# Kernel tuning notes

Hardware: AMD Instinct MI355X
Metric: run time of the kernel (lower is better)

Reference implementation:

```python
import jax, jax.numpy as jnp
import numpy as np

B, S, IN, H, C = 4, 1024, 1024, 256, 8

def setup_inputs() -> dict:
    key = jax.random.key(0)
    ks = jax.random.split(key, 9)
    scale_in = 1.0 / np.sqrt(IN)
    scale_h2 = 1.0 / np.sqrt(2 * H)
    return {
        "seq_feats": jax.random.normal(ks[0], (B, S, IN), dtype=jnp.float32),
        "U": jax.random.normal(ks[1], (H, C, H), dtype=jnp.float32) * 0.02,
        "W_weight": jax.random.uniform(ks[2], (C, 2 * H), minval=-scale_h2, maxval=scale_h2, dtype=jnp.float32),
        "W_bias": jax.random.uniform(ks[3], (C,), minval=-scale_h2, maxval=scale_h2, dtype=jnp.float32),
        "start_w": jax.random.uniform(ks[4], (H, IN), minval=-scale_in, maxval=scale_in, dtype=jnp.float32),
        "start_b": jax.random.uniform(ks[5], (H,), minval=-scale_in, maxval=scale_in, dtype=jnp.float32),
        "end_w": jax.random.uniform(ks[6], (H, IN), minval=-scale_in, maxval=scale_in, dtype=jnp.float32),
        "end_b": jax.random.uniform(ks[7], (H,), minval=-scale_in, maxval=scale_in, dtype=jnp.float32),
    }

def reference(seq_feats, U, W_weight, W_bias, start_w, start_b, end_w, end_b):
    # Hs, He: [b, s, h]
    Hs = jnp.einsum('bsi,hi->bsh', seq_feats, start_w) + start_b
    He = jnp.einsum('bsi,hi->bsh', seq_feats, end_w) + end_b
    # biaffine: [b, s, e, c]
    biaff = jnp.einsum('bsh,hcg,beg->bsec', Hs, U, He)
    # Linear over concat([Hs_repeat, He_repeat]) == split-weight broadcast sum
    Ws, We = W_weight[:, :256], W_weight[:, 256:]
    lin = (jnp.einsum('bsh,ch->bsc', Hs, Ws)[:, :, None, :]
           + jnp.einsum('beh,ch->bec', He, We)[:, None, :, :]
           + W_bias)
    return biaff + lin
```

## Files before the change

### kernel.cpp

```cpp
#include <hip/hip_runtime.h>
#include <stdint.h>


#define BDIM 256

typedef float f32x4 __attribute__((ext_vector_type(4)));
typedef __bf16 bf16x8 __attribute__((ext_vector_type(8)));
typedef unsigned int u32;
typedef unsigned short u16;
typedef const __attribute__((address_space(1))) u32* gas_ptr;
typedef __attribute__((address_space(3))) u32* las_ptr;

static __device__ __forceinline__ void load_lds16(const void* g, void* l) {
  __builtin_amdgcn_global_load_lds((gas_ptr)g, (las_ptr)l, 16, 0, 0);
}

static __device__ __forceinline__ u16 f32_to_bf16(float f) {
  union { float f; u32 u; } v; v.f = f;
  u32 r = v.u + 0x7FFFu + ((v.u >> 16) & 1u);
  return (u16)(r >> 16);
}
static __device__ __forceinline__ float bf16lo_to_f32(u32 u) {
  union { u32 u; float f; } v; v.u = u << 16;
  return v.f;
}
static __device__ __forceinline__ float bf16hi_to_f32(u32 u) {
  union { u32 u; float f; } v; v.u = u & 0xFFFF0000u;
  return v.f;
}

static __device__ __forceinline__ void stage32(u16* lds, int dst, const u16* src,
                                               int srow, int ld, int kcol, int tid) {
  const int r = tid >> 3;
  const int sl = tid & 7;
  load_lds16(src + (size_t)(srow + r) * ld + kcol + ((sl ^ (r & 7)) << 3),
             &lds[dst + tid * 8]);
}

static __device__ __forceinline__ bf16x8 rd64(const u16* lds, int base, int row, int kslot) {
  return *reinterpret_cast<const bf16x8*>(&lds[base + row * 64 + ((kslot ^ (row & 7)) << 3)]);
}

__global__ __launch_bounds__(BDIM, 4)
void k1(const u16* __restrict__ Xbf,
        const u16* __restrict__ wbf,
        u16* __restrict__ Hboth,
        const float* __restrict__ sb,
        const float* __restrict__ eb)
{
  __shared__ u16 lds[2 * 4096];

  const int tid  = threadIdx.x;
  const int lane = tid & 63;
  const int wv   = tid >> 6;
  const int wr   = wv >> 1;
  const int wq   = wv & 1;
  const int rA   = lane & 15;
  const int kq   = lane >> 4;

  int id = blockIdx.y * gridDim.x + blockIdx.x;
  id = (id & 7) * 64 + (id >> 3);
  const int n0 = (id & 7) * 64;
  const int m0 = (id >> 3) * 64;

  f32x4 acc[2][2];
#pragma unroll
  for (int i = 0; i < 2; ++i)
#pragma unroll
    for (int j = 0; j < 2; ++j) acc[i][j] = (f32x4)0.f;

#pragma unroll 1
  for (int kt = 0; kt < 1024; kt += 64) {
    stage32(lds, 0,        Xbf, m0,      1024, kt, tid);
    stage32(lds, 2048,     Xbf, m0 + 32, 1024, kt, tid);
    stage32(lds, 4096,     wbf, n0,      1024, kt, tid);
    stage32(lds, 4096+2048,wbf, n0 + 32, 1024, kt, tid);
    __syncthreads();

    bf16x8 aF[2][2], bF[2][2];
#pragma unroll
    for (int mi = 0; mi < 2; ++mi)
#pragma unroll
      for (int ks = 0; ks < 2; ++ks)
        aF[mi][ks] = rd64(lds, 0, wr * 32 + mi * 16 + rA, (ks << 2) | kq);
#pragma unroll
    for (int ni = 0; ni < 2; ++ni)
#pragma unroll
      for (int ks = 0; ks < 2; ++ks)
        bF[ni][ks] = rd64(lds, 4096, wq * 32 + ni * 16 + rA, (ks << 2) | kq);
#pragma unroll
    for (int mi = 0; mi < 2; ++mi)
#pragma unroll
      for (int ni = 0; ni < 2; ++ni)
#pragma unroll
        for (int ks = 0; ks < 2; ++ks)
          acc[mi][ni] = __builtin_amdgcn_mfma_f32_16x16x32_bf16(
              aF[mi][ks], bF[ni][ks], acc[mi][ni], 0, 0, 0);
    __syncthreads();
  }

#pragma unroll
  for (int mi = 0; mi < 2; ++mi) {
#pragma unroll
    for (int ni = 0; ni < 2; ++ni) {
      const int n = n0 + wq * 32 + ni * 16 + rA;
      const float bn = (n < 256) ? sb[n] : eb[n - 256];
      const int mr = m0 + wr * 32 + mi * 16 + kq * 4;
#pragma unroll
      for (int r = 0; r < 4; ++r)
        Hboth[(size_t)(mr + r) * 512 + n] = f32_to_bf16(acc[mi][ni][r] + bn);
    }
  }
}

__global__ __launch_bounds__(BDIM, 4)
void gemm128_biaff(const u16* __restrict__ Tall,
                   const u16* __restrict__ Bg,
                   float* __restrict__ Out,
                   const float* __restrict__ linSall,
                   const float* __restrict__ linEall)
{
  __shared__ u16 lds[2 * 8192];

  const int tid  = threadIdx.x;
  const int lane = tid & 63;
  const int wv   = tid >> 6;
  const int wr   = wv >> 1;
  const int wc   = wv & 1;
  const int rA   = lane & 15;
  const int kq   = lane >> 4;
  const int z    = blockIdx.z;

  int id = blockIdx.y * gridDim.x + blockIdx.x;
  id = (id & 7) * 64 + (id >> 3);
  const int n0 = (id & 7) * 128;
  const int m0 = (id >> 3) * 128;

  const u16* Ag  = Tall + (size_t)z * (8192 * 256);
  const u16* Bgz = Bg   + (size_t)z * (1024 * 512);

  f32x4 acc[4][4];
#pragma unroll
  for (int i = 0; i < 4; ++i)
#pragma unroll
    for (int j = 0; j < 4; ++j) acc[i][j] = (f32x4)0.f;

#pragma unroll 1
  for (int kt = 0; kt < 256; kt += 64) {
#pragma unroll
    for (int h = 0; h < 4; ++h)
      stage32(lds, h * 2048, Ag, m0 + h * 32, 256, kt, tid);
#pragma unroll
    for (int h = 0; h < 4; ++h)
      stage32(lds, 8192 + h * 2048, Bgz, n0 + h * 32, 512, kt, tid);
    __syncthreads();

    bf16x8 aF[4][2], bF[4][2];
#pragma unroll
    for (int mi = 0; mi < 4; ++mi)
#pragma unroll
      for (int ks = 0; ks < 2; ++ks)
        aF[mi][ks] = rd64(lds, 0, wr * 64 + mi * 16 + rA, (ks << 2) | kq);
#pragma unroll
    for (int ni = 0; ni < 4; ++ni)
#pragma unroll
      for (int ks = 0; ks < 2; ++ks)
        bF[ni][ks] = rd64(lds, 8192, wc * 64 + ni * 16 + rA, (ks << 2) | kq);
#pragma unroll
    for (int mi = 0; mi < 4; ++mi)
#pragma unroll
      for (int ni = 0; ni < 4; ++ni)
#pragma unroll
        for (int ks = 0; ks < 2; ++ks)
          acc[mi][ni] = __builtin_amdgcn_mfma_f32_16x16x32_bf16(
              aF[mi][ks], bF[ni][ks], acc[mi][ni], 0, 0, 0);
    __syncthreads();
  }

  float* OutZ = Out + (size_t)z * 8388608;
  const float* lS = linSall + (size_t)z * 8192;
  const float* lE = linEall + (size_t)z * 8192;
#pragma unroll
  for (int mi = 0; mi < 4; ++mi) {
#pragma unroll
    for (int ni = 0; ni < 4; ++ni) {
      const int mBase = m0 + wr * 64 + mi * 16 + kq * 4;
      const int e = n0 + wc * 64 + ni * 16 + rA;
      const int s = mBase >> 3;
      const int c0 = mBase & 7;
      const float4 ls4 = *reinterpret_cast<const float4*>(lS + mBase);
      const float4 le4 = *reinterpret_cast<const float4*>(lE + (e << 3) + c0);
      float4 o;
      o.x = acc[mi][ni][0] + ls4.x + le4.x;
      o.y = acc[mi][ni][1] + ls4.y + le4.y;
      o.z = acc[mi][ni][2] + ls4.z + le4.z;
      o.w = acc[mi][ni][3] + ls4.w + le4.w;
      *reinterpret_cast<float4*>(OutZ + ((size_t)s << 13) + ((size_t)e << 3) + c0) = o;
    }
  }
}

__global__ __launch_bounds__(BDIM, 2)
void k2lin(const u16* __restrict__ Hboth,
           const u16* __restrict__ Utbf,
           u16* __restrict__ Tbf,
           const float* __restrict__ Ww,
           const float* __restrict__ Wb,
           float* __restrict__ linS,
           float* __restrict__ linE)
{
  const int bid = blockIdx.x;
  const int tid = threadIdx.x;

  if (bid >= 512) {
    const int idx = (bid - 512) * BDIM + tid;
    const int m = idx >> 3;
    const int c = idx & 7;
    const uint4* hs4 = reinterpret_cast<const uint4*>(Hboth + (size_t)m * 512);
    const uint4* he4 = reinterpret_cast<const uint4*>(Hboth + (size_t)m * 512 + 256);
    const float* wsp = Ww + c * 512;
    const float* wep = wsp + 256;
    float s1 = 0.f, s2 = 0.f;
#pragma unroll 4
    for (int t = 0; t < 32; ++t) {
      const uint4 a = hs4[t];
      const uint4 b = he4[t];
      const u32 aw[4] = {a.x, a.y, a.z, a.w};
      const u32 bw[4] = {b.x, b.y, b.z, b.w};
#pragma unroll
      for (int q = 0; q < 4; ++q) {
        const int h = t * 8 + q * 2;
        s1 += bf16lo_to_f32(aw[q]) * wsp[h] + bf16hi_to_f32(aw[q]) * wsp[h + 1];
        s2 += bf16lo_to_f32(bw[q]) * wep[h] + bf16hi_to_f32(bw[q]) * wep[h + 1];
      }
    }
    linS[idx] = s1;
    linE[idx] = s2 + Wb[c];
    return;
  }

  __shared__ u16 lsA[128 * 32];
  __shared__ u16 lsB[128 * 32];

  int id = bid;
  id = (id & 7) * 64 + (id >> 3);
  const int n0 = (id & 15) * 128;
  const int m0 = (id >> 4) * 128;

  const int lane = tid & 63;
  const int wv   = tid >> 6;
  const int wr   = wv >> 1;
  const int wc   = wv & 1;
  const int rA   = lane & 15;
  const int ko   = (lane >> 4) * 8;

  f32x4 acc[4][4];
#pragma unroll
  for (int i = 0; i < 4; ++i)
#pragma unroll
    for (int j = 0; j < 4; ++j) acc[i][j] = (f32x4)0.f;

  for (int kt = 0; kt < 256; kt += 32) {
#pragma unroll
    for (int it = 0; it < 2; ++it) {
      const int chunk = it * BDIM + tid;
      const int row = chunk >> 2;
      const int ce = (chunk & 3) * 8;
      load_lds16(Hboth + (size_t)(m0 + row) * 512 + (kt + ce), &lsA[chunk * 8]);
      load_lds16(Utbf + (size_t)(n0 + row) * 256 + (kt + ce), &lsB[chunk * 8]);
    }
    __syncthreads();

    bf16x8 aF[4], bF[4];
#pragma unroll
    for (int i = 0; i < 4; ++i)
      aF[i] = *reinterpret_cast<const bf16x8*>(&lsA[(wr * 64 + i * 16 + rA) * 32 + ko]);
#pragma unroll
    for (int j = 0; j < 4; ++j)
      bF[j] = *reinterpret_cast<const bf16x8*>(&lsB[(wc * 64 + j * 16 + rA) * 32 + ko]);
#pragma unroll
    for (int i = 0; i < 4; ++i)
#pragma unroll
      for (int j = 0; j < 4; ++j)
        acc[i][j] = __builtin_amdgcn_mfma_f32_16x16x32_bf16(aF[i], bF[j], acc[i][j], 0, 0, 0);
    __syncthreads();
  }

  const int rgr = (lane >> 4) * 4;
#pragma unroll
  for (int i = 0; i < 4; ++i) {
#pragma unroll
    for (int j = 0; j < 4; ++j) {
      const int mBase = m0 + wr * 64 + i * 16 + rgr;
      const int n = n0 + wc * 64 + j * 16 + rA;
#pragma unroll
      for (int r = 0; r < 4; ++r)
        Tbf[(size_t)(mBase + r) * 2048 + n] = f32_to_bf16(acc[i][j][r]);
    }
  }
}

__global__ void prep_kernel(const float* __restrict__ seq,
                            const float* __restrict__ sw,
                            const float* __restrict__ ew,
                            const float* __restrict__ U,
                            u16* __restrict__ Xbf,
                            u16* __restrict__ wbf,
                            u16* __restrict__ Ut)
{
  const int bid = blockIdx.x;
  const int tid = threadIdx.x;
  if (bid < 4096) {
    const int i = bid * 1024 + tid * 4;
    const float4 v = *reinterpret_cast<const float4*>(seq + i);
    ushort4 o;
    o.x = f32_to_bf16(v.x); o.y = f32_to_bf16(v.y);
    o.z = f32_to_bf16(v.z); o.w = f32_to_bf16(v.w);
    *reinterpret_cast<ushort4*>(Xbf + i) = o;
  } else if (bid < 4608) {
    const int i = (bid - 4096) * 1024 + tid * 4;
    const float* src = (i < 262144) ? (sw + i) : (ew + (i - 262144));
    const float4 v = *reinterpret_cast<const float4*>(src);
    ushort4 o;
    o.x = f32_to_bf16(v.x); o.y = f32_to_bf16(v.y);
    o.z = f32_to_bf16(v.z); o.w = f32_to_bf16(v.w);
    *reinterpret_cast<ushort4*>(wbf + i) = o;
  } else {
    const int i = (bid - 4608) * 1024 + tid * 4;
    const int n = i >> 8;
    const int h = i & 255;
    ushort4 o;
    o.x = f32_to_bf16(U[(size_t)(h + 0) * 2048 + n]);
    o.y = f32_to_bf16(U[(size_t)(h + 1) * 2048 + n]);
    o.z = f32_to_bf16(U[(size_t)(h + 2) * 2048 + n]);
    o.w = f32_to_bf16(U[(size_t)(h + 3) * 2048 + n]);
    *reinterpret_cast<ushort4*>(Ut + i) = o;
  }
}

extern "C" void kernel_launch(void* const* d_in, const int* in_sizes, int n_in,
                              void* d_out, int out_size, void* d_ws, size_t ws_size,
                              hipStream_t stream)
{
  const float* seq = (const float*)d_in[0];
  const float* U   = (const float*)d_in[1];
  const float* Ww  = (const float*)d_in[2];
  const float* Wb  = (const float*)d_in[3];
  const float* sw  = (const float*)d_in[4];
  const float* sb  = (const float*)d_in[5];
  const float* ew  = (const float*)d_in[6];
  const float* eb  = (const float*)d_in[7];
  float* out = (float*)d_out;

  u16* Xbf   = (u16*)d_ws;
  u16* wbf   = Xbf  + 4194304;
  u16* Utbf  = wbf  + 524288;
  u16* Hboth = Utbf + 524288;
  u16* Tbf   = Hboth + 2097152;
  float* linS = (float*)(Tbf + 8388608);
  float* linE = linS + 32768;

  prep_kernel<<<5120, BDIM, 0, stream>>>(seq, sw, ew, U, Xbf, wbf, Utbf);

  k1<<<dim3(8, 64, 1), BDIM, 0, stream>>>(Xbf, wbf, Hboth, sb, eb);

  k2lin<<<640, BDIM, 0, stream>>>(Hboth, Utbf, Tbf, Ww, Wb, linS, linE);

  gemm128_biaff<<<dim3(8, 64, 4), BDIM, 0, stream>>>(
      Tbf, Hboth + 256, out, linS, linE);
}
```

Baseline: 85.19 us.

## Fuse fp32-to-bf16 conversion into projection GEMM and restage k2 tiles

Removes the separate prep kernel. The projection GEMM now reads fp32 seq and weights directly, converting them to bf16 as it stages them into LDS, and the U transpose runs in extra blocks of the same launch. The biaffine intermediate GEMM in k2lin switches to 64-wide K tiles with the swizzled LDS layout. This saves a full write and re-read of the bf16 copy of seq plus one launch. In exchange, the staging path now uses synchronous register loads plus conversion instead of asynchronous global-to-LDS loads, and each block re-reads fp32 data at twice the byte count.

```diff
diff --git a/kernel.cpp b/kernel.cpp
--- a/kernel.cpp
+++ b/kernel.cpp
@@ -20,6 +20,9 @@
   u32 r = v.u + 0x7FFFu + ((v.u >> 16) & 1u);
   return (u16)(r >> 16);
 }
+static __device__ __forceinline__ u32 pack_bf16(float lo, float hi) {
+  return (u32)f32_to_bf16(lo) | ((u32)f32_to_bf16(hi) << 16);
+}
 static __device__ __forceinline__ float bf16lo_to_f32(u32 u) {
   union { u32 u; float f; } v; v.u = u << 16;
   return v.f;
@@ -37,20 +40,53 @@
              &lds[dst + tid * 8]);
 }
 
+static __device__ __forceinline__ void stage32_f32(u16* lds, int dst, const float* src,
+                                                   int srow, int ld, int kcol, int tid) {
+  const int r = tid >> 3;
+  const int sl = tid & 7;
+  const float* p = src + (size_t)(srow + r) * ld + kcol + ((sl ^ (r & 7)) << 3);
+  const float4 v0 = *reinterpret_cast<const float4*>(p);
+  const float4 v1 = *reinterpret_cast<const float4*>(p + 4);
+  uint4 w;
+  w.x = pack_bf16(v0.x, v0.y);
+  w.y = pack_bf16(v0.z, v0.w);
+  w.z = pack_bf16(v1.x, v1.y);
+  w.w = pack_bf16(v1.z, v1.w);
+  *reinterpret_cast<uint4*>(&lds[dst + tid * 8]) = w;
+}
+
 static __device__ __forceinline__ bf16x8 rd64(const u16* lds, int base, int row, int kslot) {
   return *reinterpret_cast<const bf16x8*>(&lds[base + row * 64 + ((kslot ^ (row & 7)) << 3)]);
 }
 
 __global__ __launch_bounds__(BDIM, 4)
-void k1(const u16* __restrict__ Xbf,
-        const u16* __restrict__ wbf,
-        u16* __restrict__ Hboth,
-        const float* __restrict__ sb,
-        const float* __restrict__ eb)
+void k1p(const float* __restrict__ seq,
+         const float* __restrict__ sw,
+         const float* __restrict__ ew,
+         const float* __restrict__ U,
+         const float* __restrict__ sb,
+         const float* __restrict__ eb,
+         u16* __restrict__ Hboth,
+         u16* __restrict__ Ut)
 {
+  const int tid = threadIdx.x;
+  const int bid = blockIdx.x;
+
+  if (bid >= 512) {
+    const int i = (bid - 512) * 1024 + tid * 4;
+    const int n = i >> 8;
+    const int h = i & 255;
+    ushort4 o;
+    o.x = f32_to_bf16(U[(size_t)(h + 0) * 2048 + n]);
+    o.y = f32_to_bf16(U[(size_t)(h + 1) * 2048 + n]);
+    o.z = f32_to_bf16(U[(size_t)(h + 2) * 2048 + n]);
+    o.w = f32_to_bf16(U[(size_t)(h + 3) * 2048 + n]);
+    *reinterpret_cast<ushort4*>(Ut + i) = o;
+    return;
+  }
+
   __shared__ u16 lds[2 * 4096];
 
-  const int tid  = threadIdx.x;
   const int lane = tid & 63;
   const int wv   = tid >> 6;
   const int wr   = wv >> 1;
@@ -58,11 +94,14 @@
   const int rA   = lane & 15;
   const int kq   = lane >> 4;
 
-  int id = blockIdx.y * gridDim.x + blockIdx.x;
+  int id = bid;
   id = (id & 7) * 64 + (id >> 3);
   const int n0 = (id & 7) * 64;
   const int m0 = (id >> 3) * 64;
 
+  const float* wsrc = (n0 < 256) ? (sw + (size_t)n0 * 1024)
+                                 : (ew + (size_t)(n0 - 256) * 1024);
+
   f32x4 acc[2][2];
 #pragma unroll
   for (int i = 0; i < 2; ++i)
@@ -71,10 +110,10 @@
 
 #pragma unroll 1
   for (int kt = 0; kt < 1024; kt += 64) {
-    stage32(lds, 0,        Xbf, m0,      1024, kt, tid);
-    stage32(lds, 2048,     Xbf, m0 + 32, 1024, kt, tid);
-    stage32(lds, 4096,     wbf, n0,      1024, kt, tid);
-    stage32(lds, 4096+2048,wbf, n0 + 32, 1024, kt, tid);
+    stage32_f32(lds, 0,           seq,  m0,      1024, kt, tid);
+    stage32_f32(lds, 2048,        seq,  m0 + 32, 1024, kt, tid);
+    stage32_f32(lds, 4096,        wsrc, 0,       1024, kt, tid);
+    stage32_f32(lds, 4096 + 2048, wsrc, 32,      1024, kt, tid);
     __syncthreads();
 
     bf16x8 aF[2][2], bF[2][2];
@@ -109,93 +148,6 @@
 #pragma unroll
       for (int r = 0; r < 4; ++r)
         Hboth[(size_t)(mr + r) * 512 + n] = f32_to_bf16(acc[mi][ni][r] + bn);
-    }
-  }
-}
-
-__global__ __launch_bounds__(BDIM, 4)
-void gemm128_biaff(const u16* __restrict__ Tall,
-                   const u16* __restrict__ Bg,
-                   float* __restrict__ Out,
-                   const float* __restrict__ linSall,
-                   const float* __restrict__ linEall)
-{
-  __shared__ u16 lds[2 * 8192];
-
-  const int tid  = threadIdx.x;
-  const int lane = tid & 63;
-  const int wv   = tid >> 6;
-  const int wr   = wv >> 1;
-  const int wc   = wv & 1;
-  const int rA   = lane & 15;
-  const int kq   = lane >> 4;
-  const int z    = blockIdx.z;
-
-  int id = blockIdx.y * gridDim.x + blockIdx.x;
-  id = (id & 7) * 64 + (id >> 3);
-  const int n0 = (id & 7) * 128;
-  const int m0 = (id >> 3) * 128;
-
-  const u16* Ag  = Tall + (size_t)z * (8192 * 256);
-  const u16* Bgz = Bg   + (size_t)z * (1024 * 512);
-
-  f32x4 acc[4][4];
-#pragma unroll
-  for (int i = 0; i < 4; ++i)
-#pragma unroll
-    for (int j = 0; j < 4; ++j) acc[i][j] = (f32x4)0.f;
-
-#pragma unroll 1
-  for (int kt = 0; kt < 256; kt += 64) {
-#pragma unroll
-    for (int h = 0; h < 4; ++h)
-      stage32(lds, h * 2048, Ag, m0 + h * 32, 256, kt, tid);
-#pragma unroll
-    for (int h = 0; h < 4; ++h)
-      stage32(lds, 8192 + h * 2048, Bgz, n0 + h * 32, 512, kt, tid);
-    __syncthreads();
-
-    bf16x8 aF[4][2], bF[4][2];
-#pragma unroll
-    for (int mi = 0; mi < 4; ++mi)
-#pragma unroll
-      for (int ks = 0; ks < 2; ++ks)
-        aF[mi][ks] = rd64(lds, 0, wr * 64 + mi * 16 + rA, (ks << 2) | kq);
-#pragma unroll
-    for (int ni = 0; ni < 4; ++ni)
-#pragma unroll
-      for (int ks = 0; ks < 2; ++ks)
-        bF[ni][ks] = rd64(lds, 8192, wc * 64 + ni * 16 + rA, (ks << 2) | kq);
-#pragma unroll
-    for (int mi = 0; mi < 4; ++mi)
-#pragma unroll
-      for (int ni = 0; ni < 4; ++ni)
-#pragma unroll
-        for (int ks = 0; ks < 2; ++ks)
-          acc[mi][ni] = __builtin_amdgcn_mfma_f32_16x16x32_bf16(
-              aF[mi][ks], bF[ni][ks], acc[mi][ni], 0, 0, 0);
-    __syncthreads();
-  }
-
-  float* OutZ = Out + (size_t)z * 8388608;
-  const float* lS = linSall + (size_t)z * 8192;
-  const float* lE = linEall + (size_t)z * 8192;
-#pragma unroll
-  for (int mi = 0; mi < 4; ++mi) {
-#pragma unroll
-    for (int ni = 0; ni < 4; ++ni) {
-      const int mBase = m0 + wr * 64 + mi * 16 + kq * 4;
-      const int e = n0 + wc * 64 + ni * 16 + rA;
-      const int s = mBase >> 3;
-      const int c0 = mBase & 7;
-      const float4 ls4 = *reinterpret_cast<const float4*>(lS + mBase);
-      const float4 le4 = *reinterpret_cast<const float4*>(lE + (e << 3) + c0);
-      float4 o;
-      o.x = acc[mi][ni][0] + ls4.x + le4.x;
-      o.y = acc[mi][ni][1] + ls4.y + le4.y;
-      o.z = acc[mi][ni][2] + ls4.z + le4.z;
-      o.w = acc[mi][ni][3] + ls4.w + le4.w;
-      *reinterpret_cast<float4*>(OutZ + ((size_t)s << 13) + ((size_t)e << 3) + c0) = o;
     }
   }
 }
@@ -239,8 +191,7 @@
     return;
   }
 
-  __shared__ u16 lsA[128 * 32];
-  __shared__ u16 lsB[128 * 32];
+  __shared__ u16 lds[2 * 8192];
 
   int id = bid;
   id = (id & 7) * 64 + (id >> 3);
@@ -252,7 +203,7 @@
   const int wr   = wv >> 1;
   const int wc   = wv & 1;
   const int rA   = lane & 15;
-  const int ko   = (lane >> 4) * 8;
+  const int kq   = lane >> 4;
 
   f32x4 acc[4][4];
 #pragma unroll
@@ -260,81 +211,135 @@
 #pragma unroll
     for (int j = 0; j < 4; ++j) acc[i][j] = (f32x4)0.f;
 
-  for (int kt = 0; kt < 256; kt += 32) {
-#pragma unroll
-    for (int it = 0; it < 2; ++it) {
-      const int chunk = it * BDIM + tid;
-      const int row = chunk >> 2;
-      const int ce = (chunk & 3) * 8;
-      load_lds16(Hboth + (size_t)(m0 + row) * 512 + (kt + ce), &lsA[chunk * 8]);
-      load_lds16(Utbf + (size_t)(n0 + row) * 256 + (kt + ce), &lsB[chunk * 8]);
+#pragma unroll 1
+  for (int kt = 0; kt < 256; kt += 64) {
+#pragma unroll
+    for (int h = 0; h < 4; ++h)
+      stage32(lds, h * 2048, Hboth, m0 + h * 32, 512, kt, tid);
+#pragma unroll
+    for (int h = 0; h < 4; ++h)
+      stage32(lds, 8192 + h * 2048, Utbf, n0 + h * 32, 256, kt, tid);
+    __syncthreads();
+
+    bf16x8 aF[4][2], bF[4][2];
+#pragma unroll
+    for (int mi = 0; mi < 4; ++mi)
+#pragma unroll
+      for (int ks = 0; ks < 2; ++ks)
+        aF[mi][ks] = rd64(lds, 0, wr * 64 + mi * 16 + rA, (ks << 2) | kq);
+#pragma unroll
+    for (int ni = 0; ni < 4; ++ni)
+#pragma unroll
+      for (int ks = 0; ks < 2; ++ks)
+        bF[ni][ks] = rd64(lds, 8192, wc * 64 + ni * 16 + rA, (ks << 2) | kq);
+#pragma unroll
+    for (int mi = 0; mi < 4; ++mi)
+#pragma unroll
+      for (int ni = 0; ni < 4; ++ni)
+#pragma unroll
+        for (int ks = 0; ks < 2; ++ks)
+          acc[mi][ni] = __builtin_amdgcn_mfma_f32_16x16x32_bf16(
+              aF[mi][ks], bF[ni][ks], acc[mi][ni], 0, 0, 0);
+    __syncthreads();
+  }
+
+#pragma unroll
+  for (int mi = 0; mi < 4; ++mi) {
+#pragma unroll
+    for (int ni = 0; ni < 4; ++ni) {
+      const int mBase = m0 + wr * 64 + mi * 16 + kq * 4;
+      const int n = n0 + wc * 64 + ni * 16 + rA;
+#pragma unroll
+      for (int r = 0; r < 4; ++r)
+        Tbf[(size_t)(mBase + r) * 2048 + n] = f32_to_bf16(acc[mi][ni][r]);
     }
-    __syncthreads();
-
-    bf16x8 aF[4], bF[4];
-#pragma unroll
-    for (int i = 0; i < 4; ++i)
-      aF[i] = *reinterpret_cast<const bf16x8*>(&lsA[(wr * 64 + i * 16 + rA) * 32 + ko]);
-#pragma unroll
-    for (int j = 0; j < 4; ++j)
-      bF[j] = *reinterpret_cast<const bf16x8*>(&lsB[(wc * 64 + j * 16 + rA) * 32 + ko]);
-#pragma unroll
-    for (int i = 0; i < 4; ++i)
-#pragma unroll
-      for (int j = 0; j < 4; ++j)
-        acc[i][j] = __builtin_amdgcn_mfma_f32_16x16x32_bf16(aF[i], bF[j], acc[i][j], 0, 0, 0);
-    __syncthreads();
-  }
-
-  const int rgr = (lane >> 4) * 4;
-#pragma unroll
-  for (int i = 0; i < 4; ++i) {
-#pragma unroll
-    for (int j = 0; j < 4; ++j) {
-      const int mBase = m0 + wr * 64 + i * 16 + rgr;
-      const int n = n0 + wc * 64 + j * 16 + rA;
-#pragma unroll
-      for (int r = 0; r < 4; ++r)
-        Tbf[(size_t)(mBase + r) * 2048 + n] = f32_to_bf16(acc[i][j][r]);
+  }
+}
+
+__global__ __launch_bounds__(BDIM, 4)
+void gemm128_biaff(const u16* __restrict__ Tall,
+                   const u16* __restrict__ Bg,
+                   float* __restrict__ Out,
+                   const float* __restrict__ linSall,
+                   const float* __restrict__ linEall)
+{
+  __shared__ u16 lds[2 * 8192];
+
+  const int tid  = threadIdx.x;
+  const int lane = tid & 63;
+  const int wv   = tid >> 6;
+  const int wr   = wv >> 1;
+  const int wc   = wv & 1;
+  const int rA   = lane & 15;
+  const int kq   = lane >> 4;
+  const int z    = blockIdx.z;
+
+  int id = blockIdx.y * gridDim.x + blockIdx.x;
+  id = (id & 7) * 64 + (id >> 3);
+  const int n0 = (id & 7) * 128;
+  const int m0 = (id >> 3) * 128;
+
+  const u16* Ag  = Tall + (size_t)z * (8192 * 256);
+  const u16* Bgz = Bg   + (size_t)z * (1024 * 512);
+
+  f32x4 acc[4][4];
+#pragma unroll
+  for (int i = 0; i < 4; ++i)
+#pragma unroll
+    for (int j = 0; j < 4; ++j) acc[i][j] = (f32x4)0.f;
+
+#pragma unroll 1
+  for (int kt = 0; kt < 256; kt += 64) {
+#pragma unroll
+    for (int h = 0; h < 4; ++h)
+      stage32(lds, h * 2048, Ag, m0 + h * 32, 256, kt, tid);
+#pragma unroll
+    for (int h = 0; h < 4; ++h)
+      stage32(lds, 8192 + h * 2048, Bgz, n0 + h * 32, 512, kt, tid);
+    __syncthreads();
+
+    bf16x8 aF[4][2], bF[4][2];
+#pragma unroll
+    for (int mi = 0; mi < 4; ++mi)
+#pragma unroll
+      for (int ks = 0; ks < 2; ++ks)
+        aF[mi][ks] = rd64(lds, 0, wr * 64 + mi * 16 + rA, (ks << 2) | kq);
+#pragma unroll
+    for (int ni = 0; ni < 4; ++ni)
+#pragma unroll
+      for (int ks = 0; ks < 2; ++ks)
+        bF[ni][ks] = rd64(lds, 8192, wc * 64 + ni * 16 + rA, (ks << 2) | kq);
+#pragma unroll
+    for (int mi = 0; mi < 4; ++mi)
+#pragma unroll
+      for (int ni = 0; ni < 4; ++ni)
+#pragma unroll
+        for (int ks = 0; ks < 2; ++ks)
+          acc[mi][ni] = __builtin_amdgcn_mfma_f32_16x16x32_bf16(
+              aF[mi][ks], bF[ni][ks], acc[mi][ni], 0, 0, 0);
+    __syncthreads();
+  }
+
+  float* OutZ = Out + (size_t)z * 8388608;
+  const float* lS = linSall + (size_t)z * 8192;
+  const float* lE = linEall + (size_t)z * 8192;
+#pragma unroll
+  for (int mi = 0; mi < 4; ++mi) {
+#pragma unroll
+    for (int ni = 0; ni < 4; ++ni) {
+      const int mBase = m0 + wr * 64 + mi * 16 + kq * 4;
+      const int e = n0 + wc * 64 + ni * 16 + rA;
+      const int s = mBase >> 3;
+      const int c0 = mBase & 7;
+      const float4 ls4 = *reinterpret_cast<const float4*>(lS + mBase);
+      const float4 le4 = *reinterpret_cast<const float4*>(lE + (e << 3) + c0);
+      float4 o;
+      o.x = acc[mi][ni][0] + ls4.x + le4.x;
+      o.y = acc[mi][ni][1] + ls4.y + le4.y;
+      o.z = acc[mi][ni][2] + ls4.z + le4.z;
+      o.w = acc[mi][ni][3] + ls4.w + le4.w;
+      *reinterpret_cast<float4*>(OutZ + ((size_t)s << 13) + ((size_t)e << 3) + c0) = o;
     }
-  }
-}
-
-__global__ void prep_kernel(const float* __restrict__ seq,
-                            const float* __restrict__ sw,
-                            const float* __restrict__ ew,
-                            const float* __restrict__ U,
-                            u16* __restrict__ Xbf,
-                            u16* __restrict__ wbf,
-                            u16* __restrict__ Ut)
-{
-  const int bid = blockIdx.x;
-  const int tid = threadIdx.x;
-  if (bid < 4096) {
-    const int i = bid * 1024 + tid * 4;
-    const float4 v = *reinterpret_cast<const float4*>(seq + i);
-    ushort4 o;
-    o.x = f32_to_bf16(v.x); o.y = f32_to_bf16(v.y);
-    o.z = f32_to_bf16(v.z); o.w = f32_to_bf16(v.w);
-    *reinterpret_cast<ushort4*>(Xbf + i) = o;
-  } else if (bid < 4608) {
-    const int i = (bid - 4096) * 1024 + tid * 4;
-    const float* src = (i < 262144) ? (sw + i) : (ew + (i - 262144));
-    const float4 v = *reinterpret_cast<const float4*>(src);
-    ushort4 o;
-    o.x = f32_to_bf16(v.x); o.y = f32_to_bf16(v.y);
-    o.z = f32_to_bf16(v.z); o.w = f32_to_bf16(v.w);
-    *reinterpret_cast<ushort4*>(wbf + i) = o;
-  } else {
-    const int i = (bid - 4608) * 1024 + tid * 4;
-    const int n = i >> 8;
-    const int h = i & 255;
-    ushort4 o;
-    o.x = f32_to_bf16(U[(size_t)(h + 0) * 2048 + n]);
-    o.y = f32_to_bf16(U[(size_t)(h + 1) * 2048 + n]);
-    o.z = f32_to_bf16(U[(size_t)(h + 2) * 2048 + n]);
-    o.w = f32_to_bf16(U[(size_t)(h + 3) * 2048 + n]);
-    *reinterpret_cast<ushort4*>(Ut + i) = o;
   }
 }
 
@@ -352,17 +357,13 @@
   const float* eb  = (const float*)d_in[7];
   float* out = (float*)d_out;
 
-  u16* Xbf   = (u16*)d_ws;
-  u16* wbf   = Xbf  + 4194304;
-  u16* Utbf  = wbf  + 524288;
+  u16* Utbf  = (u16*)d_ws;
   u16* Hboth = Utbf + 524288;
   u16* Tbf   = Hboth + 2097152;
   float* linS = (float*)(Tbf + 8388608);
   float* linE = linS + 32768;
 
-  prep_kernel<<<5120, BDIM, 0, stream>>>(seq, sw, ew, U, Xbf, wbf, Utbf);
-
-  k1<<<dim3(8, 64, 1), BDIM, 0, stream>>>(Xbf, wbf, Hboth, sb, eb);
+  k1p<<<1024, BDIM, 0, stream>>>(seq, sw, ew, U, sb, eb, Hboth, Utbf);
 
   k2lin<<<640, BDIM, 0, stream>>>(Hboth, Utbf, Tbf, Ww, Wb, linS, linE);
 
```

New measurement: 82.20 us. 1.04x faster.
